# Kernel optimization log

Hardware: AMD Instinct MI355X
Metric: run time of the kernel (lower is better)

Reference implementation:

```python
import jax, jax.numpy as jnp
import numpy as np

DT_MIN, DT_MAX, STAB_EPS, RMS_EPS = 1e-4, 10.0, 1e-8, 1e-6


def soft_clamp(x, mn=DT_MIN, mx=DT_MAX):
    center = (mx + mn) / 2.0
    half = (mx - mn) / 2.0
    return center + half * jnp.tanh((x - center) / half)


def setup_inputs() -> dict:
    key = jax.random.key(0)
    ks = jax.random.split(key, 8)
    B, L, D, N = 1, 4096, 1024, 16
    s = D ** -0.5
    x = jax.random.normal(ks[0], (B, L, D), jnp.float32)
    # S4D-real style init: A = -exp(A_log), rows = -(1..N)
    A_log = jnp.broadcast_to(jnp.log(jnp.arange(1, N + 1, dtype=jnp.float32)), (D, N))
    W_delta = jax.random.normal(ks[1], (D, D), jnp.float32) * s
    b_delta = jax.random.normal(ks[2], (D,), jnp.float32) * 0.1
    W_B = jax.random.normal(ks[3], (D, N), jnp.float32) * s
    W_C = jax.random.normal(ks[4], (D, N), jnp.float32) * s
    D_skip = jax.random.normal(ks[5], (D,), jnp.float32) * 0.1 + 1.0
    norm_weight = jnp.ones((D,), jnp.float32)
    return {"x": x, "A_log": A_log, "W_delta": W_delta, "b_delta": b_delta,
            "W_B": W_B, "W_C": W_C, "D_skip": D_skip, "norm_weight": norm_weight}


def reference(x, A_log, W_delta, b_delta, W_B, W_C, D_skip, norm_weight):
    # RMSNorm pre-norm
    rms = jnp.sqrt(jnp.mean(x * x, axis=-1, keepdims=True) + RMS_EPS)
    xn = norm_weight * x / rms                                  # (B, L, D)

    # input-dependent (selective) parameters
    delta = soft_clamp(jax.nn.softplus(xn @ W_delta + b_delta))  # (B, L, D)
    Bp = xn @ W_B                                               # (B, L, N)
    C = xn @ W_C                                                # (B, L, N)
    A = -jnp.exp(A_log)                                         # (D, N)

    # guarded Tustin (bilinear) discretization
    half_dA = 0.5 * delta[..., None] * A                        # (B, L, D, N)
    denom_inv = 1.0 / jnp.maximum(1.0 - half_dA, STAB_EPS)
    A_bar = (1.0 + half_dA) * denom_inv                         # (B, L, D, N)
    B_bar = jnp.sqrt(delta)[..., None] * Bp[:, :, None, :] * denom_inv
    Bx = B_bar * xn[..., None]                                  # (B, L, D, N)

    # linear recurrence h_t = A_bar_t * h_{t-1} + Bx_t ; y_t = sum_n C_t * h_t
    def step(h, inp):
        a_t, bx_t, c_t = inp
        h = a_t * h + bx_t                                      # (B, D, N)
        y_t = jnp.einsum('bdn,bn->bd', h, c_t)
        return h, y_t

    h0 = jnp.zeros((x.shape[0], A.shape[0], A.shape[1]), x.dtype)
    seq = (jnp.moveaxis(A_bar, 1, 0), jnp.moveaxis(Bx, 1, 0), jnp.moveaxis(C, 1, 0))
    _, ys = jax.lax.scan(step, h0, seq)
    y = jnp.moveaxis(ys, 0, 1) + D_skip * xn                    # skip connection
    return y
```

## Files before the change

kernel.cpp:

```cpp
#include <hip/hip_runtime.h>
#include <hip/hip_fp16.h>
#include <cmath>

typedef _Float16 half8 __attribute__((ext_vector_type(8)));
typedef _Float16 half4_t __attribute__((ext_vector_type(4)));
typedef float f32x4 __attribute__((ext_vector_type(4)));

#define LDIM 4096
#define DDIM 1024
#define NSTATE 16
#define NCHUNK 128
#define CLEN 32

#define GLD16(g, l) __builtin_amdgcn_global_load_lds( \
    (const __attribute__((address_space(1))) void*)(g), \
    (__attribute__((address_space(3))) void*)(l), 16, 0, 0)

__global__ __launch_bounds__(256) void k_prep(const float* __restrict__ W,
                                              const float* __restrict__ WB,
                                              const float* __restrict__ WC,
                                              _Float16* __restrict__ Wt,
                                              _Float16* __restrict__ BCe) {
  const int t = threadIdx.x;
  if (blockIdx.x < 16) {
    __shared__ float tile[64][65];
    const int n0 = blockIdx.x * 64, k0 = blockIdx.y * 64;
#pragma unroll
    for (int i = 0; i < 16; ++i) {
      int idx = t + i * 256;
      int kk = idx >> 6, nn = idx & 63;
      tile[kk][nn] = W[(size_t)(k0 + kk) * DDIM + n0 + nn];
    }
    __syncthreads();
#pragma unroll
    for (int i = 0; i < 16; ++i) {
      int idx = t + i * 256;
      int nn = idx >> 6, kk = idx & 63;
      Wt[(size_t)(n0 + nn) * DDIM + k0 + kk] = (_Float16)tile[kk][nn];
    }
  } else {
#pragma unroll
    for (int rr = 0; rr < 2; ++rr) {
      int r = 2 * blockIdx.y + rr;
      const float* src = (r & 1) ? WC : WB;
      int n = r >> 1;
#pragma unroll
      for (int j = 0; j < 4; ++j) {
        int k = t * 4 + j;
        BCe[(size_t)r * DDIM + k] = (_Float16)src[(size_t)k * NSTATE + n];
      }
    }
  }
}

__global__ __launch_bounds__(256) void k_rmsnorm(const float* __restrict__ x,
                                                 const float* __restrict__ nw,
                                                 _Float16* __restrict__ xnh) {
  const int l = blockIdx.x, t = threadIdx.x;
  float4 v = ((const float4*)(x + (size_t)l * DDIM))[t];
  float ss = v.x * v.x + v.y * v.y + v.z * v.z + v.w * v.w;
#pragma unroll
  for (int off = 32; off; off >>= 1) ss += __shfl_xor(ss, off, 64);
  __shared__ float sred[4];
  if ((t & 63) == 0) sred[t >> 6] = ss;
  __syncthreads();
  float tot = sred[0] + sred[1] + sred[2] + sred[3];
  float r = rsqrtf(tot * (1.0f / (float)DDIM) + 1e-6f);
  float4 wv = ((const float4*)nw)[t];
  half4_t h;
  h[0] = (_Float16)(v.x * wv.x * r); h[1] = (_Float16)(v.y * wv.y * r);
  h[2] = (_Float16)(v.z * wv.z * r); h[3] = (_Float16)(v.w * wv.w * r);
  ((half4_t*)(xnh + (size_t)l * DDIM))[t] = h;
}

__global__ __launch_bounds__(256) void k_gemm(const _Float16* __restrict__ Ah,
                                              const _Float16* __restrict__ Bh,
                                              const _Float16* __restrict__ B2h,
                                              const float* __restrict__ b_delta,
                                              _Float16* __restrict__ sdh,
                                              float* __restrict__ bpp) {
  __shared__ __align__(16) _Float16 As[2][128 * 32];
  __shared__ __align__(16) _Float16 Bs[2][128 * 32];
  __shared__ __align__(16) _Float16 B2s[2][32 * 32];
  const int t = threadIdx.x;
  const int w = t >> 6, lane = t & 63;
  const int quad = lane >> 4, l16 = lane & 15;
  const int wr = w >> 1, wc = w & 1;
  const int bx = blockIdx.x, by = blockIdx.y;
  const int tileM = by * 128, tileN = bx * 128;

  const int srow = lane >> 2, scol = (lane & 3) * 8;
  const _Float16* gA0 = Ah + (size_t)(tileM + w * 32 + srow) * DDIM + scol;
  const _Float16* gB0 = Bh + (size_t)(tileN + w * 32 + srow) * DDIM + scol;
  const _Float16* gC0 = B2h + (size_t)(w * 16 + srow) * DDIM + scol;

  f32x4 acc[4][4], acc2[4];
#pragma unroll
  for (int i = 0; i < 4; ++i) {
    acc2[i] = (f32x4){0.f, 0.f, 0.f, 0.f};
#pragma unroll
    for (int j = 0; j < 4; ++j) acc[i][j] = (f32x4){0.f, 0.f, 0.f, 0.f};
  }

  auto stage = [&](int kt, int p) {
    const int ko = kt * 32;
    GLD16(gA0 + ko,              &As[p][(w * 32) * 32]);
    GLD16(gA0 + 16 * DDIM + ko,  &As[p][(w * 32 + 16) * 32]);
    GLD16(gB0 + ko,              &Bs[p][(w * 32) * 32]);
    GLD16(gB0 + 16 * DDIM + ko,  &Bs[p][(w * 32 + 16) * 32]);
    if ((kt >> 2) == bx && w < 2)
      GLD16(gC0 + ko,            &B2s[p][(w * 16) * 32]);
  };

  stage(0, 0);
  for (int kt = 0; kt < 32; ++kt) {
    const int p = kt & 1;
    __syncthreads();
    if (kt < 31) stage(kt + 1, p ^ 1);
    half8 af[4], bf[4];
#pragma unroll
    for (int i = 0; i < 4; ++i)
      af[i] = *(const half8*)&As[p][(wr * 64 + i * 16 + l16) * 32 + quad * 8];
#pragma unroll
    for (int j = 0; j < 4; ++j)
      bf[j] = *(const half8*)&Bs[p][(wc * 64 + j * 16 + l16) * 32 + quad * 8];
#pragma unroll
    for (int i = 0; i < 4; ++i)
#pragma unroll
      for (int j = 0; j < 4; ++j)
        acc[i][j] = __builtin_amdgcn_mfma_f32_16x16x32_f16(af[i], bf[j], acc[i][j], 0, 0, 0);
    if ((kt >> 2) == bx) {
      half8 cf = *(const half8*)&B2s[p][(wc * 16 + l16) * 32 + quad * 8];
#pragma unroll
      for (int i = 0; i < 4; ++i)
        acc2[i] = __builtin_amdgcn_mfma_f32_16x16x32_f16(af[i], cf, acc2[i], 0, 0, 0);
    }
  }

  const float cC = 5.00005f, cH = 4.99995f, invH = 1.0f / 4.99995f;
  float bdl[4];
#pragma unroll
  for (int j = 0; j < 4; ++j) bdl[j] = b_delta[tileN + wc * 64 + j * 16 + l16];
#pragma unroll
  for (int i = 0; i < 4; ++i) {
#pragma unroll
    for (int r = 0; r < 4; ++r) {
      int row = tileM + wr * 64 + i * 16 + quad * 4 + r;
#pragma unroll
      for (int j = 0; j < 4; ++j) {
        int col = tileN + wc * 64 + j * 16 + l16;
        float z = acc[i][j][r] + bdl[j];
        float e = __expf(-fabsf(z));
        float sp = fmaxf(z, 0.f) + __logf(1.0f + e);
        float tt = (sp - cC) * invH;
        float e2 = __expf(-2.0f * fabsf(tt));
        float th = copysignf((1.0f - e2) / (1.0f + e2), tt);
        float dt = fmaf(cH, th, cC);
        sdh[(size_t)row * DDIM + col] = (_Float16)sqrtf(dt);
      }
    }
  }
#pragma unroll
  for (int i = 0; i < 4; ++i) {
#pragma unroll
    for (int r = 0; r < 4; ++r) {
      int row = tileM + wr * 64 + i * 16 + quad * 4 + r;
      bpp[((size_t)bx * LDIM + row) * 32 + wc * 16 + l16] = acc2[i][r];
    }
  }
}

__device__ inline void load_bc(const float* __restrict__ bpp, int c, int t, float2* bcs) {
#pragma unroll
  for (int u = t; u < CLEN * NSTATE; u += 256) {
    int l = u >> 4, n2 = (u & 15) * 2;
    float bs = 0.f, cs = 0.f;
#pragma unroll
    for (int p = 0; p < 8; ++p) {
      size_t base = ((size_t)p * LDIM + c * CLEN + l) * 32;
      bs += bpp[base + n2];
      cs += bpp[base + n2 + 1];
    }
    bcs[u] = make_float2(bs, cs);
  }
}

__global__ __launch_bounds__(256) void k_scan1(const _Float16* __restrict__ sdh,
                                               const _Float16* __restrict__ xnh,
                                               const float* __restrict__ bpp,
                                               const float* __restrict__ A_log,
                                               float2* __restrict__ Ph) {
  __shared__ float2 bcs[CLEN * NSTATE];
  const int t = threadIdx.x;
  const int d = blockIdx.x * 256 + t;
  const int c = blockIdx.y;
  load_bc(bpp, c, t, bcs);
  float halfA[NSTATE], h[NSTATE], P[NSTATE];
#pragma unroll
  for (int n = 0; n < NSTATE; ++n) {
    halfA[n] = -0.5f * __expf(A_log[d * NSTATE + n]);
    h[n] = 0.f; P[n] = 1.f;
  }
  __syncthreads();
  const _Float16* sdr = sdh + (size_t)c * CLEN * DDIM + d;
  const _Float16* xr = xnh + (size_t)c * CLEN * DDIM + d;
#pragma unroll 2
  for (int i = 0; i < CLEN; ++i) {
    float sdv = (float)sdr[(size_t)i * DDIM];
    float xv = (float)xr[(size_t)i * DDIM];
    float dsq = sdv * sdv;
    float sdx = sdv * xv;
#pragma unroll
    for (int n = 0; n < NSTATE; ++n) {
      float2 bc = bcs[i * NSTATE + n];
      float hd = dsq * halfA[n];
      float di = __builtin_amdgcn_rcpf(1.0f - hd);
      float ab = fmaf(hd, di, di);
      h[n] = fmaf(ab, h[n], sdx * bc.x * di);
      P[n] *= ab;
    }
  }
#pragma unroll
  for (int n = 0; n < NSTATE; ++n)
    Ph[((size_t)c * NSTATE + n) * DDIM + d] = make_float2(P[n], h[n]);
}

__global__ __launch_bounds__(64) void k_comb(const float2* __restrict__ Ph,
                                             float* __restrict__ Hinit) {
  const int g = blockIdx.x * 64 + threadIdx.x;
  float H = 0.f;
  for (int cb = 0; cb < NCHUNK; cb += 8) {
    float2 ph[8];
#pragma unroll
    for (int u = 0; u < 8; ++u)
      ph[u] = Ph[(size_t)(cb + u) * (DDIM * NSTATE) + g];
#pragma unroll
    for (int u = 0; u < 8; ++u) {
      Hinit[(size_t)(cb + u) * (DDIM * NSTATE) + g] = H;
      H = fmaf(ph[u].x, H, ph[u].y);
    }
  }
}

__global__ __launch_bounds__(256) void k_scan2(const _Float16* __restrict__ sdh,
                                               const _Float16* __restrict__ xnh,
                                               const float* __restrict__ bpp,
                                               const float* __restrict__ A_log,
                                               const float* __restrict__ Hinit,
                                               const float* __restrict__ Dskip,
                                               float* __restrict__ y) {
  __shared__ float2 bcs[CLEN * NSTATE];
  const int t = threadIdx.x;
  const int d = blockIdx.x * 256 + t;
  const int c = blockIdx.y;
  load_bc(bpp, c, t, bcs);
  float halfA[NSTATE], h[NSTATE];
#pragma unroll
  for (int n = 0; n < NSTATE; ++n) {
    halfA[n] = -0.5f * __expf(A_log[d * NSTATE + n]);
    h[n] = Hinit[(size_t)c * (DDIM * NSTATE) + n * DDIM + d];
  }
  const float dsk = Dskip[d];
  __syncthreads();
  const _Float16* sdr = sdh + (size_t)c * CLEN * DDIM + d;
  const _Float16* xr = xnh + (size_t)c * CLEN * DDIM + d;
  float* yr = y + (size_t)c * CLEN * DDIM + d;
#pragma unroll 2
  for (int i = 0; i < CLEN; ++i) {
    float sdv = (float)sdr[(size_t)i * DDIM];
    float xv = (float)xr[(size_t)i * DDIM];
    float dsq = sdv * sdv;
    float sdx = sdv * xv;
    float acc = dsk * xv;
#pragma unroll
    for (int n = 0; n < NSTATE; ++n) {
      float2 bc = bcs[i * NSTATE + n];
      float hd = dsq * halfA[n];
      float di = __builtin_amdgcn_rcpf(1.0f - hd);
      float ab = fmaf(hd, di, di);
      h[n] = fmaf(ab, h[n], sdx * bc.x * di);
      acc = fmaf(bc.y, h[n], acc);
    }
    yr[(size_t)i * DDIM] = acc;
  }
}

extern "C" void kernel_launch(void* const* d_in, const int* in_sizes, int n_in,
                              void* d_out, int out_size, void* d_ws, size_t ws_size,
                              hipStream_t stream) {
  const float* x       = (const float*)d_in[0];
  const float* A_log   = (const float*)d_in[1];
  const float* W_delta = (const float*)d_in[2];
  const float* b_delta = (const float*)d_in[3];
  const float* W_B     = (const float*)d_in[4];
  const float* W_C     = (const float*)d_in[5];
  const float* D_skip  = (const float*)d_in[6];
  const float* norm_w  = (const float*)d_in[7];
  float* y = (float*)d_out;

  char* ws = (char*)d_ws;
  const size_t MB = 1024 * 1024;
  _Float16* xnh = (_Float16*)(ws);
  _Float16* Wt  = (_Float16*)(ws + 8 * MB);
  _Float16* BCe = (_Float16*)(ws + 10 * MB);
  _Float16* sdh = (_Float16*)(ws + 11 * MB);
  float*    bpp = (float*)(ws + 19 * MB);
  float2*   Ph  = (float2*)(ws + 23 * MB);
  float*    Hin = (float*)(ws + 39 * MB);
  (void)ws_size; (void)in_sizes; (void)n_in; (void)out_size;

  hipLaunchKernelGGL(k_prep, dim3(17, 16), dim3(256), 0, stream, W_delta, W_B, W_C, Wt, BCe);
  hipLaunchKernelGGL(k_rmsnorm, dim3(LDIM), dim3(256), 0, stream, x, norm_w, xnh);
  hipLaunchKernelGGL(k_gemm, dim3(8, 32), dim3(256), 0, stream, xnh, Wt, BCe, b_delta, sdh, bpp);
  hipLaunchKernelGGL(k_scan1, dim3(4, NCHUNK), dim3(256), 0, stream, sdh, xnh, bpp, A_log, Ph);
  hipLaunchKernelGGL(k_comb, dim3(256), dim3(64), 0, stream, Ph, Hin);
  hipLaunchKernelGGL(k_scan2, dim3(4, NCHUNK), dim3(256), 0, stream,
                     sdh, xnh, bpp, A_log, Hin, D_skip, y);
}
```

Measured before the change: 175.5 us.

## Fuse prep with RMSNorm, shrink GEMM N-tile, atomically reduce B/C projections

Merges the weight-prep and RMSNorm kernels into one launch, which also zeroes the B/C accumulation buffer. The GEMM tile narrows from 128x128 to 128x64, giving 512 blocks instead of 256 to fill more CUs, with a 2-blocks-per-SM launch bound. B/C partial sums are now accumulated with atomicAdd into one buffer rather than written as 8 partials that each scan kernel had to sum. This removes one launch and the 8-way reduction in the scans, at the cost of float atomics, non-deterministic summation order, and more A-tile reloads from the narrower tile.

```diff
diff --git a/kernel.cpp b/kernel.cpp
--- a/kernel.cpp
+++ b/kernel.cpp
@@ -16,15 +16,37 @@
     (const __attribute__((address_space(1))) void*)(g), \
     (__attribute__((address_space(3))) void*)(l), 16, 0, 0)
 
-__global__ __launch_bounds__(256) void k_prep(const float* __restrict__ W,
-                                              const float* __restrict__ WB,
-                                              const float* __restrict__ WC,
-                                              _Float16* __restrict__ Wt,
-                                              _Float16* __restrict__ BCe) {
-  const int t = threadIdx.x;
-  if (blockIdx.x < 16) {
+__global__ __launch_bounds__(256) void k_prep_norm(const float* __restrict__ x,
+                                                   const float* __restrict__ nw,
+                                                   const float* __restrict__ W,
+                                                   const float* __restrict__ WB,
+                                                   const float* __restrict__ WC,
+                                                   _Float16* __restrict__ xnh,
+                                                   _Float16* __restrict__ Wt,
+                                                   _Float16* __restrict__ BCe,
+                                                   float* __restrict__ bpc) {
+  const int b = blockIdx.x, t = threadIdx.x;
+  if (b < 4096) {
+    const int l = b;
+    if (t < 32) bpc[(size_t)l * 32 + t] = 0.f;
+    float4 v = ((const float4*)(x + (size_t)l * DDIM))[t];
+    float ss = v.x * v.x + v.y * v.y + v.z * v.z + v.w * v.w;
+#pragma unroll
+    for (int off = 32; off; off >>= 1) ss += __shfl_xor(ss, off, 64);
+    __shared__ float sred[4];
+    if ((t & 63) == 0) sred[t >> 6] = ss;
+    __syncthreads();
+    float tot = sred[0] + sred[1] + sred[2] + sred[3];
+    float r = rsqrtf(tot * (1.0f / (float)DDIM) + 1e-6f);
+    float4 wv = ((const float4*)nw)[t];
+    half4_t h;
+    h[0] = (_Float16)(v.x * wv.x * r); h[1] = (_Float16)(v.y * wv.y * r);
+    h[2] = (_Float16)(v.z * wv.z * r); h[3] = (_Float16)(v.w * wv.w * r);
+    ((half4_t*)(xnh + (size_t)l * DDIM))[t] = h;
+  } else if (b < 4352) {
     __shared__ float tile[64][65];
-    const int n0 = blockIdx.x * 64, k0 = blockIdx.y * 64;
+    const int bb = b - 4096;
+    const int n0 = (bb & 15) * 64, k0 = (bb >> 4) * 64;
 #pragma unroll
     for (int i = 0; i < 16; ++i) {
       int idx = t + i * 256;
@@ -39,9 +61,10 @@
       Wt[(size_t)(n0 + nn) * DDIM + k0 + kk] = (_Float16)tile[kk][nn];
     }
   } else {
+    const int by2 = b - 4352;
 #pragma unroll
     for (int rr = 0; rr < 2; ++rr) {
-      int r = 2 * blockIdx.y + rr;
+      int r = 2 * by2 + rr;
       const float* src = (r & 1) ? WC : WB;
       int n = r >> 1;
 #pragma unroll
@@ -53,63 +76,42 @@
   }
 }
 
-__global__ __launch_bounds__(256) void k_rmsnorm(const float* __restrict__ x,
-                                                 const float* __restrict__ nw,
-                                                 _Float16* __restrict__ xnh) {
-  const int l = blockIdx.x, t = threadIdx.x;
-  float4 v = ((const float4*)(x + (size_t)l * DDIM))[t];
-  float ss = v.x * v.x + v.y * v.y + v.z * v.z + v.w * v.w;
-#pragma unroll
-  for (int off = 32; off; off >>= 1) ss += __shfl_xor(ss, off, 64);
-  __shared__ float sred[4];
-  if ((t & 63) == 0) sred[t >> 6] = ss;
-  __syncthreads();
-  float tot = sred[0] + sred[1] + sred[2] + sred[3];
-  float r = rsqrtf(tot * (1.0f / (float)DDIM) + 1e-6f);
-  float4 wv = ((const float4*)nw)[t];
-  half4_t h;
-  h[0] = (_Float16)(v.x * wv.x * r); h[1] = (_Float16)(v.y * wv.y * r);
-  h[2] = (_Float16)(v.z * wv.z * r); h[3] = (_Float16)(v.w * wv.w * r);
-  ((half4_t*)(xnh + (size_t)l * DDIM))[t] = h;
-}
-
-__global__ __launch_bounds__(256) void k_gemm(const _Float16* __restrict__ Ah,
-                                              const _Float16* __restrict__ Bh,
-                                              const _Float16* __restrict__ B2h,
-                                              const float* __restrict__ b_delta,
-                                              _Float16* __restrict__ sdh,
-                                              float* __restrict__ bpp) {
+__global__ __launch_bounds__(256, 2) void k_gemm64(const _Float16* __restrict__ Ah,
+                                                   const _Float16* __restrict__ Bh,
+                                                   const _Float16* __restrict__ B2h,
+                                                   const float* __restrict__ b_delta,
+                                                   _Float16* __restrict__ sdh,
+                                                   float* __restrict__ bpc) {
   __shared__ __align__(16) _Float16 As[2][128 * 32];
-  __shared__ __align__(16) _Float16 Bs[2][128 * 32];
+  __shared__ __align__(16) _Float16 Bs[2][64 * 32];
   __shared__ __align__(16) _Float16 B2s[2][32 * 32];
   const int t = threadIdx.x;
   const int w = t >> 6, lane = t & 63;
   const int quad = lane >> 4, l16 = lane & 15;
   const int wr = w >> 1, wc = w & 1;
-  const int bx = blockIdx.x, by = blockIdx.y;
-  const int tileM = by * 128, tileN = bx * 128;
-
+  const int bid = blockIdx.x;
+  const int bx = bid & 15, by = bid >> 4;
+  const int tileM = by * 128, tileN = bx * 64;
   const int srow = lane >> 2, scol = (lane & 3) * 8;
   const _Float16* gA0 = Ah + (size_t)(tileM + w * 32 + srow) * DDIM + scol;
-  const _Float16* gB0 = Bh + (size_t)(tileN + w * 32 + srow) * DDIM + scol;
+  const _Float16* gB0 = Bh + (size_t)(tileN + w * 16 + srow) * DDIM + scol;
   const _Float16* gC0 = B2h + (size_t)(w * 16 + srow) * DDIM + scol;
 
-  f32x4 acc[4][4], acc2[4];
+  f32x4 acc[4][2], acc2[4];
 #pragma unroll
   for (int i = 0; i < 4; ++i) {
     acc2[i] = (f32x4){0.f, 0.f, 0.f, 0.f};
 #pragma unroll
-    for (int j = 0; j < 4; ++j) acc[i][j] = (f32x4){0.f, 0.f, 0.f, 0.f};
+    for (int j = 0; j < 2; ++j) acc[i][j] = (f32x4){0.f, 0.f, 0.f, 0.f};
   }
 
   auto stage = [&](int kt, int p) {
     const int ko = kt * 32;
-    GLD16(gA0 + ko,              &As[p][(w * 32) * 32]);
-    GLD16(gA0 + 16 * DDIM + ko,  &As[p][(w * 32 + 16) * 32]);
-    GLD16(gB0 + ko,              &Bs[p][(w * 32) * 32]);
-    GLD16(gB0 + 16 * DDIM + ko,  &Bs[p][(w * 32 + 16) * 32]);
-    if ((kt >> 2) == bx && w < 2)
-      GLD16(gC0 + ko,            &B2s[p][(w * 16) * 32]);
+    GLD16(gA0 + ko,             &As[p][(w * 32) * 32]);
+    GLD16(gA0 + 16 * DDIM + ko, &As[p][(w * 32 + 16) * 32]);
+    GLD16(gB0 + ko,             &Bs[p][(w * 16) * 32]);
+    if ((kt >> 1) == bx && w < 2)
+      GLD16(gC0 + ko,           &B2s[p][(w * 16) * 32]);
   };
 
   stage(0, 0);
@@ -117,19 +119,19 @@
     const int p = kt & 1;
     __syncthreads();
     if (kt < 31) stage(kt + 1, p ^ 1);
-    half8 af[4], bf[4];
+    half8 af[4], bf[2];
 #pragma unroll
     for (int i = 0; i < 4; ++i)
       af[i] = *(const half8*)&As[p][(wr * 64 + i * 16 + l16) * 32 + quad * 8];
 #pragma unroll
-    for (int j = 0; j < 4; ++j)
-      bf[j] = *(const half8*)&Bs[p][(wc * 64 + j * 16 + l16) * 32 + quad * 8];
+    for (int j = 0; j < 2; ++j)
+      bf[j] = *(const half8*)&Bs[p][(wc * 32 + j * 16 + l16) * 32 + quad * 8];
 #pragma unroll
     for (int i = 0; i < 4; ++i)
 #pragma unroll
-      for (int j = 0; j < 4; ++j)
+      for (int j = 0; j < 2; ++j)
         acc[i][j] = __builtin_amdgcn_mfma_f32_16x16x32_f16(af[i], bf[j], acc[i][j], 0, 0, 0);
-    if ((kt >> 2) == bx) {
+    if ((kt >> 1) == bx) {
       half8 cf = *(const half8*)&B2s[p][(wc * 16 + l16) * 32 + quad * 8];
 #pragma unroll
       for (int i = 0; i < 4; ++i)
@@ -138,17 +140,17 @@
   }
 
   const float cC = 5.00005f, cH = 4.99995f, invH = 1.0f / 4.99995f;
-  float bdl[4];
-#pragma unroll
-  for (int j = 0; j < 4; ++j) bdl[j] = b_delta[tileN + wc * 64 + j * 16 + l16];
+  float bdl[2];
+#pragma unroll
+  for (int j = 0; j < 2; ++j) bdl[j] = b_delta[tileN + wc * 32 + j * 16 + l16];
 #pragma unroll
   for (int i = 0; i < 4; ++i) {
 #pragma unroll
     for (int r = 0; r < 4; ++r) {
       int row = tileM + wr * 64 + i * 16 + quad * 4 + r;
 #pragma unroll
-      for (int j = 0; j < 4; ++j) {
-        int col = tileN + wc * 64 + j * 16 + l16;
+      for (int j = 0; j < 2; ++j) {
+        int col = tileN + wc * 32 + j * 16 + l16;
         float z = acc[i][j][r] + bdl[j];
         float e = __expf(-fabsf(z));
         float sp = fmaxf(z, 0.f) + __logf(1.0f + e);
@@ -158,43 +160,25 @@
         float dt = fmaf(cH, th, cC);
         sdh[(size_t)row * DDIM + col] = (_Float16)sqrtf(dt);
       }
-    }
-  }
-#pragma unroll
-  for (int i = 0; i < 4; ++i) {
-#pragma unroll
-    for (int r = 0; r < 4; ++r) {
-      int row = tileM + wr * 64 + i * 16 + quad * 4 + r;
-      bpp[((size_t)bx * LDIM + row) * 32 + wc * 16 + l16] = acc2[i][r];
-    }
-  }
-}
-
-__device__ inline void load_bc(const float* __restrict__ bpp, int c, int t, float2* bcs) {
-#pragma unroll
-  for (int u = t; u < CLEN * NSTATE; u += 256) {
-    int l = u >> 4, n2 = (u & 15) * 2;
-    float bs = 0.f, cs = 0.f;
-#pragma unroll
-    for (int p = 0; p < 8; ++p) {
-      size_t base = ((size_t)p * LDIM + c * CLEN + l) * 32;
-      bs += bpp[base + n2];
-      cs += bpp[base + n2 + 1];
-    }
-    bcs[u] = make_float2(bs, cs);
+      atomicAdd(&bpc[(size_t)row * 32 + wc * 16 + l16], acc2[i][r]);
+    }
   }
 }
 
 __global__ __launch_bounds__(256) void k_scan1(const _Float16* __restrict__ sdh,
                                                const _Float16* __restrict__ xnh,
-                                               const float* __restrict__ bpp,
+                                               const float* __restrict__ bpc,
                                                const float* __restrict__ A_log,
                                                float2* __restrict__ Ph) {
   __shared__ float2 bcs[CLEN * NSTATE];
   const int t = threadIdx.x;
   const int d = blockIdx.x * 256 + t;
   const int c = blockIdx.y;
-  load_bc(bpp, c, t, bcs);
+#pragma unroll
+  for (int u = t; u < CLEN * NSTATE; u += 256) {
+    int l = u >> 4, n2 = (u & 15) * 2;
+    bcs[u] = *(const float2*)&bpc[(size_t)(c * CLEN + l) * 32 + n2];
+  }
   float halfA[NSTATE], h[NSTATE], P[NSTATE];
 #pragma unroll
   for (int n = 0; n < NSTATE; ++n) {
@@ -244,7 +228,7 @@
 
 __global__ __launch_bounds__(256) void k_scan2(const _Float16* __restrict__ sdh,
                                                const _Float16* __restrict__ xnh,
-                                               const float* __restrict__ bpp,
+                                               const float* __restrict__ bpc,
                                                const float* __restrict__ A_log,
                                                const float* __restrict__ Hinit,
                                                const float* __restrict__ Dskip,
@@ -253,7 +237,11 @@
   const int t = threadIdx.x;
   const int d = blockIdx.x * 256 + t;
   const int c = blockIdx.y;
-  load_bc(bpp, c, t, bcs);
+#pragma unroll
+  for (int u = t; u < CLEN * NSTATE; u += 256) {
+    int l = u >> 4, n2 = (u & 15) * 2;
+    bcs[u] = *(const float2*)&bpc[(size_t)(c * CLEN + l) * 32 + n2];
+  }
   float halfA[NSTATE], h[NSTATE];
 #pragma unroll
   for (int n = 0; n < NSTATE; ++n) {
@@ -304,16 +292,18 @@
   _Float16* Wt  = (_Float16*)(ws + 8 * MB);
   _Float16* BCe = (_Float16*)(ws + 10 * MB);
   _Float16* sdh = (_Float16*)(ws + 11 * MB);
-  float*    bpp = (float*)(ws + 19 * MB);
-  float2*   Ph  = (float2*)(ws + 23 * MB);
-  float*    Hin = (float*)(ws + 39 * MB);
+  float*    bpc = (float*)(ws + 19 * MB);
+  float2*   Ph  = (float2*)(ws + 20 * MB);
+  float*    Hin = (float*)(ws + 36 * MB);
   (void)ws_size; (void)in_sizes; (void)n_in; (void)out_size;
 
-  hipLaunchKernelGGL(k_prep, dim3(17, 16), dim3(256), 0, stream, W_delta, W_B, W_C, Wt, BCe);
-  hipLaunchKernelGGL(k_rmsnorm, dim3(LDIM), dim3(256), 0, stream, x, norm_w, xnh);
-  hipLaunchKernelGGL(k_gemm, dim3(8, 32), dim3(256), 0, stream, xnh, Wt, BCe, b_delta, sdh, bpp);
-  hipLaunchKernelGGL(k_scan1, dim3(4, NCHUNK), dim3(256), 0, stream, sdh, xnh, bpp, A_log, Ph);
+  hipLaunchKernelGGL(k_prep_norm, dim3(4368), dim3(256), 0, stream,
+                     x, norm_w, W_delta, W_B, W_C, xnh, Wt, BCe, bpc);
+  hipLaunchKernelGGL(k_gemm64, dim3(512), dim3(256), 0, stream,
+                     xnh, Wt, BCe, b_delta, sdh, bpc);
+  hipLaunchKernelGGL(k_scan1, dim3(4, NCHUNK), dim3(256), 0, stream,
+                     sdh, xnh, bpc, A_log, Ph);
   hipLaunchKernelGGL(k_comb, dim3(256), dim3(64), 0, stream, Ph, Hin);
   hipLaunchKernelGGL(k_scan2, dim3(4, NCHUNK), dim3(256), 0, stream,
-                     sdh, xnh, bpp, A_log, Hin, D_skip, y);
-}
+                     sdh, xnh, bpc, A_log, Hin, D_skip, y);
+}
```

Result: faster. 167.1 us (-4.8%).
